# Optimization experiments

Measured on AMD Instinct MI355X. Metric: run time of the kernel, lower is better.

The kernel has to match this reference:

```python
import jax, jax.numpy as jnp
import numpy as np

N, F, H, FO = 4096, 512, 4, 128  # nodes, in-feat, heads, out-feat per head
NEG_INF = -1e10
LRELU_ALPHA = 0.2


def setup_inputs() -> dict:
    key = jax.random.key(0)
    k_x, k_a, k_w, k_as, k_an = jax.random.split(key, 5)
    X = jax.random.normal(k_x, (N, F), dtype=jnp.float32)
    A = (jax.random.uniform(k_a, (N, N)) < 0.01).astype(jnp.float32)
    A = jnp.minimum(A + jnp.eye(N, dtype=jnp.float32), 1.0)
    W = jax.random.normal(k_w, (H, F, FO), dtype=jnp.float32) * 0.05       # per-head kernels
    b = jnp.zeros((H, FO), dtype=jnp.float32)                               # per-head biases
    a_self = jax.random.normal(k_as, (H, FO), dtype=jnp.float32) * 0.05    # attn_kernel_self (F_,1) per head
    a_neigh = jax.random.normal(k_an, (H, FO), dtype=jnp.float32) * 0.05   # attn_kernel_neigh (F_,1) per head
    return {"X": X, "A": A, "W": W, "b": b, "a_self": a_self, "a_neigh": a_neigh}


def reference(X, A, W, b, a_self, a_neigh):
    # features[h] = X @ W[h] -> [H, N, FO]
    feats = jnp.einsum('nf,hfo->hno', X, W)
    # Nx1 self / neighbor scores per head -> [H, N]
    e_s = jnp.einsum('hno,ho->hn', feats, a_self)
    e_n = jnp.einsum('hno,ho->hn', feats, a_neigh)
    # broadcast-add to [H, N, N], LeakyReLU(0.2), additive adjacency mask
    logits = e_s[:, :, None] + e_n[:, None, :]
    logits = jnp.where(logits > 0, logits, LRELU_ALPHA * logits)
    logits = logits + NEG_INF * (1.0 - A)[None, :, :]
    attn = jax.nn.softmax(logits, axis=-1)          # [H, N, N]
    out = jnp.einsum('hnm,hmo->hno', attn, feats)   # weighted aggregate
    out = out + b[:, None, :]
    # concat heads: [N, H*FO]
    out = jnp.transpose(out, (1, 0, 2)).reshape(X.shape[0], -1)
    return jax.nn.relu(out)
```

## Files before the change

### kernel.cpp

```cpp
#include <hip/hip_runtime.h>
#include <math.h>

#define NODES 4096
#define FIN   512
#define HEADS 4
#define FOUT  128
#define COLS  512

__global__ __launch_bounds__(256) void gemm_feats(
    const float* __restrict__ X, const float* __restrict__ W, float* __restrict__ feats)
{
    const int tid = threadIdx.x;
    const int colBase = blockIdx.x * 64;
    const int rowBase = blockIdx.y * 64;
    const int h     = colBase >> 7;
    const int obase = colBase & 127;

    __shared__ float As[32][68];
    __shared__ float Bs[32][64];

    const int tx = tid & 15;
    const int ty = tid >> 4;

    float acc[4][4];
    #pragma unroll
    for (int i = 0; i < 4; i++)
        #pragma unroll
        for (int j = 0; j < 4; j++) acc[i][j] = 0.f;

    for (int k0 = 0; k0 < FIN; k0 += 32) {
        #pragma unroll
        for (int p = 0; p < 2; p++) {
            int v = tid + p * 256;
            int m = v >> 3, kk4 = (v & 7) * 4;
            const float4 x4 = *(const float4*)(X + (size_t)(rowBase + m) * FIN + k0 + kk4);
            As[kk4 + 0][m] = x4.x; As[kk4 + 1][m] = x4.y;
            As[kk4 + 2][m] = x4.z; As[kk4 + 3][m] = x4.w;
        }
        #pragma unroll
        for (int p = 0; p < 2; p++) {
            int v = tid + p * 256;
            int kk = v >> 4, n4 = (v & 15) * 4;
            int f = k0 + kk;
            const float4 w4 = *(const float4*)(W + ((size_t)(h * FIN + f) * FOUT) + obase + n4);
            *(float4*)&Bs[kk][n4] = w4;
        }
        __syncthreads();
        #pragma unroll
        for (int kk = 0; kk < 32; kk++) {
            float4 a4 = *(const float4*)&As[kk][ty * 4];
            float4 b4 = *(const float4*)&Bs[kk][tx * 4];
            float av[4] = {a4.x, a4.y, a4.z, a4.w};
            float bv[4] = {b4.x, b4.y, b4.z, b4.w};
            #pragma unroll
            for (int i = 0; i < 4; i++)
                #pragma unroll
                for (int j = 0; j < 4; j++)
                    acc[i][j] = fmaf(av[i], bv[j], acc[i][j]);
        }
        __syncthreads();
    }
    #pragma unroll
    for (int i = 0; i < 4; i++) {
        int r = rowBase + ty * 4 + i;
        *(float4*)(feats + (size_t)r * COLS + colBase + tx * 4) =
            make_float4(acc[i][0], acc[i][1], acc[i][2], acc[i][3]);
    }
}

__global__ __launch_bounds__(64) void scores(
    const float* __restrict__ feats, const float* __restrict__ a_self,
    const float* __restrict__ a_neigh, float* __restrict__ e_s, float* __restrict__ e_n)
{
    const int n = blockIdx.x;
    const int l = threadIdx.x;
    float ps[HEADS], pn[HEADS];
    #pragma unroll
    for (int hh = 0; hh < HEADS; hh++) {
        float x0 = feats[(size_t)n * COLS + hh * FOUT + l];
        float x1 = feats[(size_t)n * COLS + hh * FOUT + l + 64];
        ps[hh] = x0 * a_self[hh * FOUT + l]  + x1 * a_self[hh * FOUT + l + 64];
        pn[hh] = x0 * a_neigh[hh * FOUT + l] + x1 * a_neigh[hh * FOUT + l + 64];
    }
    #pragma unroll
    for (int off = 32; off > 0; off >>= 1) {
        #pragma unroll
        for (int hh = 0; hh < HEADS; hh++) {
            ps[hh] += __shfl_xor(ps[hh], off, 64);
            pn[hh] += __shfl_xor(pn[hh], off, 64);
        }
    }
    if (l == 0) {
        #pragma unroll
        for (int hh = 0; hh < HEADS; hh++) {
            e_s[hh * NODES + n] = ps[hh];
            e_n[hh * NODES + n] = pn[hh];
        }
    }
}

__global__ __launch_bounds__(256) void aggregate(
    const float* __restrict__ A, const float* __restrict__ feats,
    const float* __restrict__ e_s, const float* __restrict__ e_n,
    const float* __restrict__ bias, float* __restrict__ out)
{
    const int i = blockIdx.x;
    const int tid = threadIdx.x;
    __shared__ int   s_idx[NODES];
    __shared__ int   s_cnt;
    __shared__ float s_m[HEADS], s_d[HEADS];
    if (tid == 0) s_cnt = 0;
    __syncthreads();

    const float4* Arow = (const float4*)(A + (size_t)i * NODES);
    for (int q = tid; q < NODES / 4; q += 256) {
        float4 a = Arow[q];
        int j = q * 4;
        if (a.x != 0.f) { int p = atomicAdd(&s_cnt, 1); s_idx[p] = j; }
        if (a.y != 0.f) { int p = atomicAdd(&s_cnt, 1); s_idx[p] = j + 1; }
        if (a.z != 0.f) { int p = atomicAdd(&s_cnt, 1); s_idx[p] = j + 2; }
        if (a.w != 0.f) { int p = atomicAdd(&s_cnt, 1); s_idx[p] = j + 3; }
    }
    __syncthreads();
    const int cnt = s_cnt;

    {
        const int wv = tid >> 6;
        const int lane = tid & 63;
        const float esi = e_s[wv * NODES + i];
        float m = -1e30f;
        for (int k = lane; k < cnt; k += 64) {
            int j = s_idx[k];
            float e = esi + e_n[wv * NODES + j];
            float l = e > 0.f ? e : 0.2f * e;
            m = fmaxf(m, l);
        }
        #pragma unroll
        for (int off = 32; off > 0; off >>= 1) m = fmaxf(m, __shfl_xor(m, off, 64));
        float d = 0.f;
        for (int k = lane; k < cnt; k += 64) {
            int j = s_idx[k];
            float e = esi + e_n[wv * NODES + j];
            float l = e > 0.f ? e : 0.2f * e;
            d += __expf(l - m);
        }
        #pragma unroll
        for (int off = 32; off > 0; off >>= 1) d += __shfl_xor(d, off, 64);
        if (lane == 0) { s_m[wv] = m; s_d[wv] = d; }
    }
    __syncthreads();

    const int c0 = tid, c1 = tid + 256;
    const int h0 = c0 >> 7, h1 = c1 >> 7;
    const float es0 = e_s[h0 * NODES + i], es1 = e_s[h1 * NODES + i];
    const float m0 = s_m[h0], m1 = s_m[h1];
    float acc0 = 0.f, acc1 = 0.f;
    for (int k = 0; k < cnt; k++) {
        int j = s_idx[k];
        float en0 = e_n[h0 * NODES + j], en1 = e_n[h1 * NODES + j];
        float l0 = es0 + en0; l0 = l0 > 0.f ? l0 : 0.2f * l0;
        float l1 = es1 + en1; l1 = l1 > 0.f ? l1 : 0.2f * l1;
        float w0 = __expf(l0 - m0), w1 = __expf(l1 - m1);
        acc0 = fmaf(w0, feats[(size_t)j * COLS + c0], acc0);
        acc1 = fmaf(w1, feats[(size_t)j * COLS + c1], acc1);
    }
    float o0 = acc0 / s_d[h0] + bias[h0 * FOUT + (c0 & 127)];
    float o1 = acc1 / s_d[h1] + bias[h1 * FOUT + (c1 & 127)];
    out[(size_t)i * COLS + c0] = o0 > 0.f ? o0 : 0.f;
    out[(size_t)i * COLS + c1] = o1 > 0.f ? o1 : 0.f;
}

extern "C" void kernel_launch(void* const* d_in, const int* in_sizes, int n_in,
                              void* d_out, int out_size, void* d_ws, size_t ws_size,
                              hipStream_t stream) {
    const float* X       = (const float*)d_in[0];
    const float* A       = (const float*)d_in[1];
    const float* W       = (const float*)d_in[2];
    const float* b       = (const float*)d_in[3];
    const float* a_self  = (const float*)d_in[4];
    const float* a_neigh = (const float*)d_in[5];
    float* out = (float*)d_out;

    float* feats = (float*)d_ws;
    float* e_s   = feats + (size_t)NODES * COLS;
    float* e_n   = e_s + HEADS * NODES;

    dim3 gA(COLS / 64, NODES / 64);
    gemm_feats<<<gA, 256, 0, stream>>>(X, W, feats);
    scores<<<NODES, 64, 0, stream>>>(feats, a_self, a_neigh, e_s, e_n);
    aggregate<<<NODES, 256, 0, stream>>>(A, feats, e_s, e_n, b, out);
}
```

Before: 173.6 us.

## Use split-bf16 MFMA GEMM and precompute softmax weights in shared memory

Replaces the FP32 SIMT feature GEMM with a bf16x3 split (hi/lo) MFMA GEMM, which needs a new conversion kernel that splits X and transposes W into hi/lo bf16 buffers. The aggregate kernel now computes the exp attention weights once per head into shared memory, in chunks of 512 neighbors, and folds the denominator sum into the same pass. This removes the separate denominator pass and the redundant per-thread exp work in the inner loop. It adds an extra kernel launch, more workspace traffic for the converted operands, and slightly lower precision from dropping the lo*lo term.

```diff
diff --git a/kernel.cpp b/kernel.cpp
--- a/kernel.cpp
+++ b/kernel.cpp
@@ -7,64 +7,95 @@
 #define FOUT  128
 #define COLS  512
 
-__global__ __launch_bounds__(256) void gemm_feats(
-    const float* __restrict__ X, const float* __restrict__ W, float* __restrict__ feats)
-{
+typedef short  short8  __attribute__((ext_vector_type(8)));
+typedef float  floatx4 __attribute__((ext_vector_type(4)));
+
+__device__ inline void split2(float x, short& hi, short& lo) {
+    unsigned xb = __float_as_uint(x);
+    unsigned hb = xb & 0xFFFF0000u;
+    float hf = __uint_as_float(hb);
+    float r  = x - hf;
+    hi = (short)(hb >> 16);
+    lo = (short)(__float_as_uint(r) >> 16);
+}
+
+__global__ __launch_bounds__(256) void convert_split(
+    const float* __restrict__ X, const float* __restrict__ W,
+    short* __restrict__ Xhi, short* __restrict__ Xlo,
+    short* __restrict__ Wthi, short* __restrict__ Wtlo)
+{
+    int t = blockIdx.x * 256 + threadIdx.x;
+    const int NX = NODES * FIN;
+    const int stride = gridDim.x * 256;
+    for (int i = t; i < NX; i += stride) {
+        short hi, lo; split2(X[i], hi, lo);
+        Xhi[i] = hi; Xlo[i] = lo;
+    }
+    const int NW = HEADS * FIN * FOUT;
+    for (int i = t; i < NW; i += stride) {
+        int h = i >> 16;
+        int f = (i >> 7) & (FIN - 1);
+        int o = i & (FOUT - 1);
+        short hi, lo; split2(W[i], hi, lo);
+        size_t dst = (size_t)(h * FOUT + o) * FIN + f;
+        Wthi[dst] = hi; Wtlo[dst] = lo;
+    }
+}
+
+__global__ __launch_bounds__(256) void gemm_mfma(
+    const short* __restrict__ Xhi, const short* __restrict__ Xlo,
+    const short* __restrict__ Bthi, const short* __restrict__ Btlo,
+    float* __restrict__ feats)
+{
+    __shared__ short Ah[64][40], Al[64][40], Bh[64][40], Bl[64][40];
     const int tid = threadIdx.x;
+    const int rowBase = blockIdx.y * 64;
     const int colBase = blockIdx.x * 64;
-    const int rowBase = blockIdx.y * 64;
-    const int h     = colBase >> 7;
-    const int obase = colBase & 127;
-
-    __shared__ float As[32][68];
-    __shared__ float Bs[32][64];
-
-    const int tx = tid & 15;
-    const int ty = tid >> 4;
-
-    float acc[4][4];
-    #pragma unroll
-    for (int i = 0; i < 4; i++)
-        #pragma unroll
-        for (int j = 0; j < 4; j++) acc[i][j] = 0.f;
+    const int lane = tid & 63, w = tid >> 6;
+    const int quad = lane >> 4, lk = quad * 8, lm = lane & 15;
+
+    floatx4 acc[4];
+    #pragma unroll
+    for (int mi = 0; mi < 4; mi++) acc[mi] = (floatx4)0.f;
+
+    const int sr = tid >> 2;
+    const int sk = (tid & 3) * 8;
 
     for (int k0 = 0; k0 < FIN; k0 += 32) {
-        #pragma unroll
-        for (int p = 0; p < 2; p++) {
-            int v = tid + p * 256;
-            int m = v >> 3, kk4 = (v & 7) * 4;
-            const float4 x4 = *(const float4*)(X + (size_t)(rowBase + m) * FIN + k0 + kk4);
-            As[kk4 + 0][m] = x4.x; As[kk4 + 1][m] = x4.y;
-            As[kk4 + 2][m] = x4.z; As[kk4 + 3][m] = x4.w;
-        }
-        #pragma unroll
-        for (int p = 0; p < 2; p++) {
-            int v = tid + p * 256;
-            int kk = v >> 4, n4 = (v & 15) * 4;
-            int f = k0 + kk;
-            const float4 w4 = *(const float4*)(W + ((size_t)(h * FIN + f) * FOUT) + obase + n4);
-            *(float4*)&Bs[kk][n4] = w4;
-        }
-        __syncthreads();
-        #pragma unroll
-        for (int kk = 0; kk < 32; kk++) {
-            float4 a4 = *(const float4*)&As[kk][ty * 4];
-            float4 b4 = *(const float4*)&Bs[kk][tx * 4];
-            float av[4] = {a4.x, a4.y, a4.z, a4.w};
-            float bv[4] = {b4.x, b4.y, b4.z, b4.w};
-            #pragma unroll
-            for (int i = 0; i < 4; i++)
-                #pragma unroll
-                for (int j = 0; j < 4; j++)
-                    acc[i][j] = fmaf(av[i], bv[j], acc[i][j]);
-        }
-        __syncthreads();
-    }
-    #pragma unroll
-    for (int i = 0; i < 4; i++) {
-        int r = rowBase + ty * 4 + i;
-        *(float4*)(feats + (size_t)r * COLS + colBase + tx * 4) =
-            make_float4(acc[i][0], acc[i][1], acc[i][2], acc[i][3]);
+        const float4 ah = *(const float4*)(Xhi  + (size_t)(rowBase + sr) * FIN + k0 + sk);
+        const float4 al = *(const float4*)(Xlo  + (size_t)(rowBase + sr) * FIN + k0 + sk);
+        const float4 bh = *(const float4*)(Bthi + (size_t)(colBase + sr) * FIN + k0 + sk);
+        const float4 bl = *(const float4*)(Btlo + (size_t)(colBase + sr) * FIN + k0 + sk);
+        __syncthreads();
+        *(float4*)&Ah[sr][sk] = ah;
+        *(float4*)&Al[sr][sk] = al;
+        *(float4*)&Bh[sr][sk] = bh;
+        *(float4*)&Bl[sr][sk] = bl;
+        __syncthreads();
+
+        short8 afh[4], afl[4];
+        #pragma unroll
+        for (int mi = 0; mi < 4; mi++) {
+            afh[mi] = *(const short8*)&Ah[mi * 16 + lm][lk];
+            afl[mi] = *(const short8*)&Al[mi * 16 + lm][lk];
+        }
+        short8 bfh = *(const short8*)&Bh[w * 16 + lm][lk];
+        short8 bfl = *(const short8*)&Bl[w * 16 + lm][lk];
+        #pragma unroll
+        for (int mi = 0; mi < 4; mi++) {
+            acc[mi] = __builtin_amdgcn_mfma_f32_16x16x32_bf16(afh[mi], bfh, acc[mi], 0, 0, 0);
+            acc[mi] = __builtin_amdgcn_mfma_f32_16x16x32_bf16(afh[mi], bfl, acc[mi], 0, 0, 0);
+            acc[mi] = __builtin_amdgcn_mfma_f32_16x16x32_bf16(afl[mi], bfh, acc[mi], 0, 0, 0);
+        }
+    }
+    #pragma unroll
+    for (int mi = 0; mi < 4; mi++) {
+        #pragma unroll
+        for (int r = 0; r < 4; r++) {
+            int row = rowBase + mi * 16 + quad * 4 + r;
+            int col = colBase + w * 16 + lm;
+            feats[(size_t)row * COLS + col] = acc[mi][r];
+        }
     }
 }
 
@@ -107,8 +138,9 @@
     const int i = blockIdx.x;
     const int tid = threadIdx.x;
     __shared__ int   s_idx[NODES];
+    __shared__ float s_w[HEADS][512];
     __shared__ int   s_cnt;
-    __shared__ float s_m[HEADS], s_d[HEADS];
+    __shared__ float s_dinv[HEADS];
     if (tid == 0) s_cnt = 0;
     __syncthreads();
 
@@ -116,58 +148,54 @@
     for (int q = tid; q < NODES / 4; q += 256) {
         float4 a = Arow[q];
         int j = q * 4;
-        if (a.x != 0.f) { int p = atomicAdd(&s_cnt, 1); s_idx[p] = j; }
-        if (a.y != 0.f) { int p = atomicAdd(&s_cnt, 1); s_idx[p] = j + 1; }
-        if (a.z != 0.f) { int p = atomicAdd(&s_cnt, 1); s_idx[p] = j + 2; }
-        if (a.w != 0.f) { int p = atomicAdd(&s_cnt, 1); s_idx[p] = j + 3; }
+        if (a.x != 0.f) s_idx[atomicAdd(&s_cnt, 1)] = j;
+        if (a.y != 0.f) s_idx[atomicAdd(&s_cnt, 1)] = j + 1;
+        if (a.z != 0.f) s_idx[atomicAdd(&s_cnt, 1)] = j + 2;
+        if (a.w != 0.f) s_idx[atomicAdd(&s_cnt, 1)] = j + 3;
     }
     __syncthreads();
     const int cnt = s_cnt;
 
-    {
-        const int wv = tid >> 6;
-        const int lane = tid & 63;
-        const float esi = e_s[wv * NODES + i];
-        float m = -1e30f;
-        for (int k = lane; k < cnt; k += 64) {
-            int j = s_idx[k];
-            float e = esi + e_n[wv * NODES + j];
-            float l = e > 0.f ? e : 0.2f * e;
-            m = fmaxf(m, l);
-        }
-        #pragma unroll
-        for (int off = 32; off > 0; off >>= 1) m = fmaxf(m, __shfl_xor(m, off, 64));
-        float d = 0.f;
-        for (int k = lane; k < cnt; k += 64) {
-            int j = s_idx[k];
-            float e = esi + e_n[wv * NODES + j];
-            float l = e > 0.f ? e : 0.2f * e;
-            d += __expf(l - m);
-        }
-        #pragma unroll
-        for (int off = 32; off > 0; off >>= 1) d += __shfl_xor(d, off, 64);
-        if (lane == 0) { s_m[wv] = m; s_d[wv] = d; }
-    }
-    __syncthreads();
+    const int wv = tid >> 6, lane = tid & 63;
+    const float esi = e_s[wv * NODES + i];
+
+    float m = -1e30f;
+    for (int k = lane; k < cnt; k += 64) {
+        float e = esi + e_n[wv * NODES + s_idx[k]];
+        m = fmaxf(m, e > 0.f ? e : 0.2f * e);
+    }
+    #pragma unroll
+    for (int off = 32; off > 0; off >>= 1) m = fmaxf(m, __shfl_xor(m, off, 64));
 
     const int c0 = tid, c1 = tid + 256;
     const int h0 = c0 >> 7, h1 = c1 >> 7;
-    const float es0 = e_s[h0 * NODES + i], es1 = e_s[h1 * NODES + i];
-    const float m0 = s_m[h0], m1 = s_m[h1];
-    float acc0 = 0.f, acc1 = 0.f;
-    for (int k = 0; k < cnt; k++) {
-        int j = s_idx[k];
-        float en0 = e_n[h0 * NODES + j], en1 = e_n[h1 * NODES + j];
-        float l0 = es0 + en0; l0 = l0 > 0.f ? l0 : 0.2f * l0;
-        float l1 = es1 + en1; l1 = l1 > 0.f ? l1 : 0.2f * l1;
-        float w0 = __expf(l0 - m0), w1 = __expf(l1 - m1);
-        acc0 = fmaf(w0, feats[(size_t)j * COLS + c0], acc0);
-        acc1 = fmaf(w1, feats[(size_t)j * COLS + c1], acc1);
-    }
-    float o0 = acc0 / s_d[h0] + bias[h0 * FOUT + (c0 & 127)];
-    float o1 = acc1 / s_d[h1] + bias[h1 * FOUT + (c1 & 127)];
-    out[(size_t)i * COLS + c0] = o0 > 0.f ? o0 : 0.f;
-    out[(size_t)i * COLS + c1] = o1 > 0.f ? o1 : 0.f;
+    float acc0 = 0.f, acc1 = 0.f, d = 0.f;
+    for (int base = 0; base < cnt; base += 512) {
+        int nc = min(512, cnt - base);
+        __syncthreads();
+        for (int k = lane; k < nc; k += 64) {
+            float e = esi + e_n[wv * NODES + s_idx[base + k]];
+            float l = e > 0.f ? e : 0.2f * e;
+            float wgt = __expf(l - m);
+            s_w[wv][k] = wgt;
+            d += wgt;
+        }
+        __syncthreads();
+        for (int k = 0; k < nc; k++) {
+            size_t off = (size_t)s_idx[base + k] * COLS;
+            acc0 = fmaf(s_w[h0][k], feats[off + c0], acc0);
+            acc1 = fmaf(s_w[h1][k], feats[off + c1], acc1);
+        }
+    }
+    #pragma unroll
+    for (int off = 32; off > 0; off >>= 1) d += __shfl_xor(d, off, 64);
+    if (lane == 0) s_dinv[wv] = 1.f / d;
+    __syncthreads();
+
+    float o0 = acc0 * s_dinv[h0] + bias[h0 * FOUT + (c0 & 127)];
+    float o1 = acc1 * s_dinv[h1] + bias[h1 * FOUT + (c1 & 127)];
+    out[(size_t)i * COLS + c0] = fmaxf(o0, 0.f);
+    out[(size_t)i * COLS + c1] = fmaxf(o1, 0.f);
 }
 
 extern "C" void kernel_launch(void* const* d_in, const int* in_sizes, int n_in,
@@ -184,9 +212,14 @@
     float* feats = (float*)d_ws;
     float* e_s   = feats + (size_t)NODES * COLS;
     float* e_n   = e_s + HEADS * NODES;
-
+    short* Xhi   = (short*)(e_n + HEADS * NODES);
+    short* Xlo   = Xhi + (size_t)NODES * FIN;
+    short* Wthi  = Xlo + (size_t)NODES * FIN;
+    short* Wtlo  = Wthi + (size_t)COLS * FIN;
+
+    convert_split<<<2048, 256, 0, stream>>>(X, W, Xhi, Xlo, Wthi, Wtlo);
     dim3 gA(COLS / 64, NODES / 64);
-    gemm_feats<<<gA, 256, 0, stream>>>(X, W, feats);
+    gemm_mfma<<<gA, 256, 0, stream>>>(Xhi, Xlo, Wthi, Wtlo, feats);
     scores<<<NODES, 64, 0, stream>>>(feats, a_self, a_neigh, e_s, e_n);
     aggregate<<<NODES, 256, 0, stream>>>(A, feats, e_s, e_n, b, out);
 }
```

Result: faster. 162.4 us (-6.5%).
